# Kernel optimization log

Measured on AMD Instinct MI355X. Metric: run time of the kernel, lower is better.

The kernel has to match this reference:

```python
import jax, jax.numpy as jnp
import numpy as np
import math

NUM_SECTORS = 8
HIDDEN = 128
FEAT = 64
MAX_DIST = 10.0


def gru_last(x, Wih, Whh, bih, bhh):
    # PyTorch GRU (gate order r,z,n); x: (B,T,D) -> last hidden (B,H)
    B = x.shape[0]
    H = Whh.shape[1]
    xp = jnp.einsum('btd,gd->btg', x, Wih) + bih  # (B,T,3H)

    def step(h, xpt):
        hp = h @ Whh.T + bhh
        xr, xz, xn = jnp.split(xpt, 3, -1)
        hr, hz, hn = jnp.split(hp, 3, -1)
        r = jax.nn.sigmoid(xr + hr)
        z = jax.nn.sigmoid(xz + hz)
        n = jnp.tanh(xn + r * hn)
        h_new = (1.0 - z) * n + z * h
        return h_new, None

    h0 = jnp.zeros((B, H), x.dtype)
    hT, _ = jax.lax.scan(step, h0, jnp.swapaxes(xp, 0, 1))
    return hT


def setup_inputs() -> dict:
    key = jax.random.key(0)
    ks = iter(jax.random.split(key, 32))
    B, N, T = 2048, 64, 8
    H, Hn = HIDDEN, HIDDEN // 2
    s = 0.05

    def p(shape):
        return jax.random.normal(next(ks), shape, jnp.float32) * s

    inp = {
        'target_trajectory': jax.random.normal(next(ks), (B, T, 2), jnp.float32),
        'neighbor_trajectories': jax.random.normal(next(ks), (B, N, T, 2), jnp.float32),
        'relative_angles': jax.random.uniform(next(ks), (B, N), jnp.float32) * (2.0 * math.pi),
        'neighbor_mask': (jax.random.uniform(next(ks), (B, N)) > 0.2).astype(jnp.float32),
        # target GRU (H=128)
        'Wih_t': p((3 * H, 2)), 'Whh_t': p((3 * H, H)), 'bih_t': p((3 * H,)), 'bhh_t': p((3 * H,)),
        # neighbor GRU (H=64)
        'Wih_n': p((3 * Hn, 2)), 'Whh_n': p((3 * Hn, Hn)), 'bih_n': p((3 * Hn,)), 'bhh_n': p((3 * Hn,)),
        # sector encoder: 68 -> 128 -> 128
        'W1': p((H, 4 + Hn)), 'b1': p((H,)), 'W2': p((H, H)), 'b2': p((H,)),
        # fusion: 1152 -> 256 -> 128 -> 64
        'Wf1': p((2 * H, H + NUM_SECTORS * H)), 'bf1': p((2 * H,)),
        'Wf2': p((H, 2 * H)), 'bf2': p((H,)),
        'Wf3': p((FEAT, H)), 'bf3': p((FEAT,)),
        'ln_g': jnp.ones((FEAT,), jnp.float32), 'ln_b': jnp.zeros((FEAT,), jnp.float32),
    }
    return inp


def reference(target_trajectory, neighbor_trajectories, relative_angles, neighbor_mask,
              Wih_t, Whh_t, bih_t, bhh_t, Wih_n, Whh_n, bih_n, bhh_n,
              W1, b1, W2, b2, Wf1, bf1, Wf2, bf2, Wf3, bf3, ln_g, ln_b):
    B, N, T, D = neighbor_trajectories.shape
    S = NUM_SECTORS

    # trajectory encoders
    target_feature = gru_last(target_trajectory, Wih_t, Whh_t, bih_t, bhh_t)  # (B,128)
    nf = gru_last(neighbor_trajectories.reshape(B * N, T, D), Wih_n, Whh_n, bih_n, bhh_n)
    nf = nf.reshape(B, N, -1)  # (B,N,64)

    # geometry
    target_pos = target_trajectory[:, -1, :]                      # (B,2)
    npos = neighbor_trajectories[:, :, -1, :]                     # (B,N,2)
    dist = jnp.linalg.norm(npos - target_pos[:, None, :], axis=-1)  # (B,N)
    vel = neighbor_trajectories[:, :, -1, :] - neighbor_trajectories[:, :, -2, :]  # (B,N,2)

    # sector assignment (vectorized segment reduce over sectors)
    sector_size = 2.0 * math.pi / S
    sid = jnp.clip((relative_angles / sector_size).astype(jnp.int32), 0, S - 1)  # (B,N)
    valid = neighbor_mask > 0
    memb = ((sid[..., None] == jnp.arange(S)) & valid[..., None]).astype(dist.dtype)  # (B,N,S)

    count = memb.sum(1)                        # (B,S)
    nonempty = count > 0
    safe = jnp.maximum(count, 1.0)
    avg_d = jnp.where(nonempty, (dist[..., None] * memb).sum(1) / safe, 0.0)  # (B,S)
    avg_v = jnp.where(nonempty[..., None], jnp.einsum('bns,bnc->bsc', memb, vel) / safe[..., None], 0.0)

    w = jnp.exp(-dist / MAX_DIST)              # (B,N)
    wm = w[..., None] * memb                   # (B,N,S)
    wsum = wm.sum(1) + 1e-8                    # (B,S)
    wfeat = jnp.einsum('bns,bnh->bsh', wm, nf) / wsum[..., None]  # (B,S,64)

    sector_feats = jnp.concatenate([count[..., None], avg_d[..., None], avg_v, wfeat], axis=-1)  # (B,S,68)

    # sector encoder MLP (dropout off / eval)
    h = jax.nn.relu(sector_feats @ W1.T + b1)
    h = jax.nn.relu(h @ W2.T + b2)             # (B,S,128)
    enc = h.reshape(B, S * HIDDEN)

    combined = jnp.concatenate([target_feature, enc], axis=-1)  # (B,1152)
    f = jax.nn.relu(combined @ Wf1.T + bf1)
    f = jax.nn.relu(f @ Wf2.T + bf2)
    f = jax.nn.relu(f @ Wf3.T + bf3)           # (B,64)

    mu = f.mean(-1, keepdims=True)
    var = ((f - mu) ** 2).mean(-1, keepdims=True)
    return (f - mu) / jnp.sqrt(var + 1e-5) * ln_g + ln_b
```

## Files before the change

### kernel.cpp

```cpp
#include <hip/hip_runtime.h>

typedef __attribute__((ext_vector_type(8))) short short8;
typedef __attribute__((ext_vector_type(4))) float f32x4;

#define SGC (-1.44269504088896341f)
#define THC ( 2.88539008177792681f)

__device__ __forceinline__ unsigned short f2bf(float f){
  unsigned u = __float_as_uint(f);
  return (unsigned short)((u + 0x7fffu + ((u >> 16) & 1u)) >> 16);
}
__device__ __forceinline__ float bf2f(unsigned short b){
  return __uint_as_float(((unsigned)b) << 16);
}
__device__ __forceinline__ unsigned f2bf_cvt(float f){
  unsigned r;
  asm("v_cvt_pk_bf16_f32 %0, %1, %1" : "=v"(r) : "v"(f));
  return r;
}
__device__ __forceinline__ unsigned f2bf_pk(float lo, float hi){
  unsigned r;
  asm("v_cvt_pk_bf16_f32 %0, %1, %2" : "=v"(r) : "v"(lo), "v"(hi));
  return r;
}

__global__ __launch_bounds__(256) void k_prep(
    const float* __restrict__ Whh_t, const float* __restrict__ W1,
    const float* __restrict__ W2,    const float* __restrict__ Wf1,
    const float* __restrict__ Wf2,   const float* __restrict__ Wf3,
    const float* __restrict__ Whh_n,
    unsigned short* __restrict__ wgt)
{
  int i = blockIdx.x * 256 + threadIdx.x;
  if (i < 49152){
    int g = i >> 7;
    float s = (g < 256) ? SGC : THC;
    wgt[i] = f2bf(Whh_t[i] * s); return;
  }
  i -= 49152;
  if (i < 12288){ int r = i / 96, c = i % 96;
    wgt[49152 + i] = (c < 68) ? f2bf(W1[r*68 + c]) : (unsigned short)0; return; }
  i -= 12288;
  if (i < 16384){ wgt[61440 + i] = f2bf(W2[i]); return; }
  i -= 16384;
  if (i < 294912){ wgt[77824 + i] = f2bf(Wf1[i]); return; }
  i -= 294912;
  if (i < 32768){ wgt[372736 + i] = f2bf(Wf2[i]); return; }
  i -= 32768;
  if (i < 8192){ wgt[405504 + i] = f2bf(Wf3[i]); return; }
  i -= 8192;
  if (i < 12288){
    int g = i >> 6;
    float s = (g < 128) ? SGC : THC;
    wgt[413696 + i] = f2bf(Whh_n[i] * s); return;
  }
}

__global__ __launch_bounds__(256, 4) void k_gru_n(
    const float* __restrict__ ttraj, const float* __restrict__ ntraj,
    const float* __restrict__ rang,  const float* __restrict__ nmask,
    const float* __restrict__ Wih_n,
    const float* __restrict__ bih_n, const float* __restrict__ bhh_n,
    const unsigned short* __restrict__ wgt,
    unsigned short* __restrict__ sf)
{
  __shared__ char smem[38912];
  const int tid = threadIdx.x;
  const int w = tid >> 6, u = (tid >> 4) & 3, c = tid & 15;
  const int b = blockIdx.x;
  const unsigned short* whhN_b = wgt + 413696;

  unsigned short* whh2 = (unsigned short*)smem;
  unsigned short* wx   = whh2 + 12288;
  unsigned short* hall = (unsigned short*)(smem + 27648);
  unsigned short* hb   = hall + w * 1152;
  unsigned* xpk = (unsigned*)(smem + 36864);
  float* pool   = (float*)(smem + 36864);

  for (int i = tid; i < 1536; i += 256){
    int nt = i >> 7, rem = i & 127;
    int hf = rem >> 6, uu = (rem >> 4) & 3, cc = rem & 15;
    *(short8*)&whh2[nt*1024 + hf*512 + (uu*16+cc)*8] =
        *(const short8*)&whhN_b[(nt*16+cc)*64 + hf*32 + uu*8];
  }
  if (tid < 192){
    int t = tid >> 4, cc = tid & 15;
    float s = (t < 8) ? SGC : THC;
    int g = (t < 4) ? (t*16 + cc) : (t < 8) ? (64 + (t-4)*16 + cc) : (128 + (t-8)*16 + cc);
    float bsum = (t < 8) ? (bih_n[g] + bhh_n[g]) : bih_n[g];
    unsigned short* p = &wx[t*128 + cc*8];
    *(short8*)p = (short8){0,0,0,0,0,0,0,0};
    p[0] = f2bf(Wih_n[g*2]   * s);
    p[1] = f2bf(Wih_n[g*2+1] * s);
    p[2] = f2bf(bsum * s);
  }
  {
    float4 v = ((const float4*)(ntraj + (size_t)b * 1024))[tid];
    int n = tid >> 2, p = (tid & 3) * 2;
    xpk[p*64 + n]       = f2bf_pk(v.x, v.y);
    xpk[(p+1)*64 + n]   = f2bf_pk(v.z, v.w);
  }
  __syncthreads();

  short8 BX[12];
#pragma unroll
  for (int t = 0; t < 12; ++t) BX[t] = *(const short8*)&wx[t*128 + c*8];

  float bh_[4];
#pragma unroll
  for (int gt = 0; gt < 4; ++gt) bh_[gt] = bhh_n[128 + gt*16 + c] * THC;

  float hcur[4][4];
#pragma unroll
  for (int gt=0; gt<4; ++gt)
#pragma unroll
    for (int q=0; q<4; ++q) hcur[gt][q] = 0.0f;

  auto gates = [&](int gt, const f32x4& aR, const f32x4& aZ, const f32x4& aN, const f32x4& aX){
#pragma unroll
    for (int q = 0; q < 4; ++q){
      float r = __builtin_amdgcn_rcpf(1.0f + __builtin_amdgcn_exp2f(aR[q]));
      float z = __builtin_amdgcn_rcpf(1.0f + __builtin_amdgcn_exp2f(aZ[q]));
      float hn = aN[q] + bh_[gt];
      float pn = __builtin_fmaf(r, hn, aX[q]);
      float E = __builtin_amdgcn_exp2f(pn);
      float n = __builtin_fmaf(-2.0f, __builtin_amdgcn_rcpf(E + 1.0f), 1.0f);
      float hnew = __builtin_fmaf(z, hcur[gt][q] - n, n);
      hcur[gt][q] = hnew;
      hb[(u*4+q)*72 + gt*16 + c] = (unsigned short)f2bf_cvt(hnew);
    }
  };

  const int lane8 = (u*16 + c) * 8;
  const f32x4 zz = {0.f,0.f,0.f,0.f};

  for (int st = 0; st < 8; ++st){
    unsigned p01 = xpk[st*64 + w*16 + c];
    bool u0 = (u == 0);
    union { unsigned ui[4]; short8 s8; } a2u;
    a2u.ui[0] = u0 ? p01 : 0u;
    a2u.ui[1] = u0 ? 0x3F80u : 0u;
    a2u.ui[2] = 0u; a2u.ui[3] = 0u;
    short8 a2 = a2u.s8;

    if (st > 0){
      short8 a0 = *(short8*)&hb[c*72 + u*8];
      short8 a1 = *(short8*)&hb[c*72 + 32 + u*8];
#pragma unroll
      for (int gt = 0; gt < 4; ++gt){
        const unsigned short* pr = whh2 + gt*1024 + lane8;
        const unsigned short* pz = whh2 + (4+gt)*1024 + lane8;
        const unsigned short* pq = whh2 + (8+gt)*1024 + lane8;
        f32x4 aR = __builtin_amdgcn_mfma_f32_16x16x32_bf16(a0, *(const short8*)pr, zz, 0,0,0);
        aR = __builtin_amdgcn_mfma_f32_16x16x32_bf16(a1, *(const short8*)(pr+512), aR, 0,0,0);
        aR = __builtin_amdgcn_mfma_f32_16x16x32_bf16(a2, BX[gt], aR, 0,0,0);
        f32x4 aZ = __builtin_amdgcn_mfma_f32_16x16x32_bf16(a0, *(const short8*)pz, zz, 0,0,0);
        aZ = __builtin_amdgcn_mfma_f32_16x16x32_bf16(a1, *(const short8*)(pz+512), aZ, 0,0,0);
        aZ = __builtin_amdgcn_mfma_f32_16x16x32_bf16(a2, BX[4+gt], aZ, 0,0,0);
        f32x4 aN = __builtin_amdgcn_mfma_f32_16x16x32_bf16(a0, *(const short8*)pq, zz, 0,0,0);
        aN = __builtin_amdgcn_mfma_f32_16x16x32_bf16(a1, *(const short8*)(pq+512), aN, 0,0,0);
        f32x4 aX = __builtin_amdgcn_mfma_f32_16x16x32_bf16(a2, BX[8+gt], zz, 0,0,0);
        gates(gt, aR, aZ, aN, aX);
      }
    } else {
#pragma unroll
      for (int gt = 0; gt < 4; ++gt){
        f32x4 aR = __builtin_amdgcn_mfma_f32_16x16x32_bf16(a2, BX[gt], zz, 0,0,0);
        f32x4 aZ = __builtin_amdgcn_mfma_f32_16x16x32_bf16(a2, BX[4+gt], zz, 0,0,0);
        f32x4 aX = __builtin_amdgcn_mfma_f32_16x16x32_bf16(a2, BX[8+gt], zz, 0,0,0);
        gates(gt, aR, aZ, zz, aX);
      }
    }
  }
  __syncthreads();

  if (tid < 64){
    int n = tid;
    const float* nb = ntraj + (size_t)b*1024 + n*16;
    float px = nb[14], py = nb[15];
    float vx = px - nb[12], vy = py - nb[13];
    float m   = nmask[(size_t)b*64 + n];
    float ang = rang[(size_t)b*64 + n];
    float tx = ttraj[(size_t)b*16 + 14], ty = ttraj[(size_t)b*16 + 15];
    float dx = px - tx, dy = py - ty;
    float dist = __builtin_amdgcn_sqrtf(dx*dx + dy*dy);
    int sid = (int)(ang / 0.78539816339744830962f);
    sid = sid < 0 ? 0 : (sid > 7 ? 7 : sid);
    bool valid = m > 0.0f;
    float wv = valid ? __builtin_amdgcn_exp2f(dist * -0.14426950408889634f) : 0.0f;
    pool[n]       = valid ? dist : 0.0f;
    pool[64 + n]  = valid ? vx   : 0.0f;
    pool[128 + n] = valid ? vy   : 0.0f;
    pool[192 + n] = wv;
    pool[256 + n] = valid ? (float)sid : -1.0f;
  }
  __syncthreads();
  if (tid < 8){
    int s = tid;
    float cnt=0.f, sd=0.f, sx=0.f, sy=0.f, sw=0.f;
    for (int n=0; n<64; ++n){
      if (pool[256+n] == (float)s){
        cnt += 1.f; sd += pool[n]; sx += pool[64+n]; sy += pool[128+n]; sw += pool[192+n];
      }
    }
    float inv = (cnt > 0.f) ? __builtin_amdgcn_rcpf(cnt) : 0.f;
    pool[320 + s] = cnt;
    pool[328 + s] = sd * inv;
    pool[336 + s] = sx * inv;
    pool[344 + s] = sy * inv;
    pool[352 + s] = __builtin_amdgcn_rcpf(sw + 1e-8f);
  }
  __syncthreads();
#pragma unroll
  for (int rep = 0; rep < 2; ++rep){
    int p = tid + rep*256;
    int s = p >> 6, h = p & 63;
    float fs = (float)s;
    float a = 0.f;
    for (int n = 0; n < 64; ++n){
      float wmv = (pool[256+n] == fs) ? pool[192+n] : 0.f;
      float nf  = bf2f(hall[(n>>4)*1152 + (n&15)*72 + h]);
      a += wmv * nf;
    }
    sf[((size_t)b*8 + s)*96 + 4 + h] = (unsigned short)f2bf_cvt(a * pool[352+s]);
  }
  if (tid < 32){
    int s = tid >> 2, cc = tid & 3;
    sf[((size_t)b*8 + s)*96 + cc] = (unsigned short)f2bf_cvt(pool[320 + cc*8 + s]);
  }
  if (tid < 224){
    int s = tid / 28, cc = 68 + tid % 28;
    sf[((size_t)b*8 + s)*96 + cc] = 0;
  }
}

__global__ __launch_bounds__(256) void k_gru_t(
    const float* __restrict__ ttraj,
    const float* __restrict__ Wih_t, const float* __restrict__ bih_t, const float* __restrict__ bhh_t,
    const unsigned short* __restrict__ wgt,
    unsigned short* __restrict__ combined)
{
  __shared__ char smem[9728];
  const int tid = threadIdx.x, w = tid >> 6, u = (tid >> 4) & 3, c = tid & 15;
  unsigned short* hb0 = (unsigned short*)smem;
  unsigned short* hb1 = (unsigned short*)(smem + 4352);
  float* xs = (float*)(smem + 8704);

  xs[tid] = ttraj[(size_t)blockIdx.x*256 + tid];

  int ntg[6];
  ntg[0] = 2*w; ntg[1] = 2*w+1;
  ntg[2] = 8+2*w; ntg[3] = 9+2*w;
  ntg[4] = 16+2*w; ntg[5] = 17+2*w;

  short8 Bf[6][4];
#pragma unroll
  for (int lt2 = 0; lt2 < 6; ++lt2){
    const unsigned short* wp = wgt + (ntg[lt2]*16 + c)*128 + u*8;
#pragma unroll
    for (int kk = 0; kk < 4; ++kk)
      Bf[lt2][kk] = *(const short8*)(wp + kk*32);
  }

  float Wr0[2],Wr1[2],BR[2],Wz0[2],Wz1[2],BZ[2],Wn0[2],Wn1[2],BI[2],BH[2];
#pragma unroll
  for (int gt = 0; gt < 2; ++gt){
    int g = w*32 + gt*16 + c;
    Wr0[gt]=Wih_t[g*2]*SGC;        Wr1[gt]=Wih_t[g*2+1]*SGC;        BR[gt]=(bih_t[g]+bhh_t[g])*SGC;
    Wz0[gt]=Wih_t[(128+g)*2]*SGC;  Wz1[gt]=Wih_t[(128+g)*2+1]*SGC;  BZ[gt]=(bih_t[128+g]+bhh_t[128+g])*SGC;
    Wn0[gt]=Wih_t[(256+g)*2]*THC;  Wn1[gt]=Wih_t[(256+g)*2+1]*THC;  BI[gt]=bih_t[256+g]*THC; BH[gt]=bhh_t[256+g]*THC;
  }
  float hcur[2][4];
#pragma unroll
  for (int gt=0; gt<2; ++gt)
#pragma unroll
    for (int q=0; q<4; ++q) hcur[gt][q] = 0.0f;
  __syncthreads();

  for (int st = 0; st < 8; ++st){
    unsigned short* rbuf = (st & 1) ? hb0 : hb1;
    unsigned short* wbuf = (st & 1) ? hb1 : hb0;
    f32x4 acc[6];
    if (st > 0){
      short8 a0 = *(short8*)&rbuf[c*136 + u*8];
      short8 a1 = *(short8*)&rbuf[c*136 + 32 + u*8];
      short8 a2 = *(short8*)&rbuf[c*136 + 64 + u*8];
      short8 a3 = *(short8*)&rbuf[c*136 + 96 + u*8];
#pragma unroll
      for (int lt2 = 0; lt2 < 6; ++lt2){
        f32x4 t = {0.f,0.f,0.f,0.f};
        t = __builtin_amdgcn_mfma_f32_16x16x32_bf16(a0, Bf[lt2][0], t, 0,0,0);
        t = __builtin_amdgcn_mfma_f32_16x16x32_bf16(a1, Bf[lt2][1], t, 0,0,0);
        t = __builtin_amdgcn_mfma_f32_16x16x32_bf16(a2, Bf[lt2][2], t, 0,0,0);
        acc[lt2] = __builtin_amdgcn_mfma_f32_16x16x32_bf16(a3, Bf[lt2][3], t, 0,0,0);
      }
    } else {
#pragma unroll
      for (int lt2 = 0; lt2 < 6; ++lt2) acc[lt2] = (f32x4){0.f,0.f,0.f,0.f};
    }
#pragma unroll
    for (int gt = 0; gt < 2; ++gt){
#pragma unroll
      for (int q = 0; q < 4; ++q){
        int sq = u*4 + q;
        float x0 = xs[sq*16 + st*2], x1 = xs[sq*16 + st*2 + 1];
        float rp = __builtin_fmaf(Wr0[gt], x0, __builtin_fmaf(Wr1[gt], x1, acc[gt][q] + BR[gt]));
        float zp = __builtin_fmaf(Wz0[gt], x0, __builtin_fmaf(Wz1[gt], x1, acc[2+gt][q] + BZ[gt]));
        float r = __builtin_amdgcn_rcpf(1.0f + __builtin_amdgcn_exp2f(rp));
        float z = __builtin_amdgcn_rcpf(1.0f + __builtin_amdgcn_exp2f(zp));
        float hnv = acc[4+gt][q] + BH[gt];
        float pn = __builtin_fmaf(Wn0[gt], x0, __builtin_fmaf(Wn1[gt], x1, __builtin_fmaf(r, hnv, BI[gt])));
        float E = __builtin_amdgcn_exp2f(pn);
        float n = __builtin_fmaf(-2.0f, __builtin_amdgcn_rcpf(E + 1.0f), 1.0f);
        float hnew = __builtin_fmaf(z, hcur[gt][q] - n, n);
        hcur[gt][q] = hnew;
        if (st < 7){
          wbuf[sq*136 + w*32 + gt*16 + c] = (unsigned short)f2bf_cvt(hnew);
        } else {
          int row = blockIdx.x*16 + sq;
          combined[(size_t)row*1152 + w*32 + gt*16 + c] = (unsigned short)f2bf_cvt(hnew);
        }
      }
    }
    if (st < 7) __syncthreads();
  }
}

__global__ __launch_bounds__(256) void k_mlp12(
    const unsigned short* __restrict__ sf,
    const unsigned short* __restrict__ wgt,
    const float* __restrict__ b1, const float* __restrict__ b2,
    unsigned short* __restrict__ combined)
{
  __shared__ char smem[18432];
  unsigned short* hb = (unsigned short*)smem + (threadIdx.x >> 6) * 2176;
  float* b1s = (float*)(smem + 17408);
  float* b2s = b1s + 128;
  const unsigned short* w1b = wgt + 49152;
  const unsigned short* w2b = wgt + 61440;
  const int tid = threadIdx.x, w = tid >> 6, u = (tid >> 4) & 3, c = tid & 15;
  if (tid < 128){ b1s[tid] = b1[tid]; b2s[tid] = b2[tid]; }
  __syncthreads();
  const int rowb = blockIdx.x * 64 + w * 16;

  f32x4 acc[8];
#pragma unroll
  for (int nt=0; nt<8; ++nt) acc[nt] = (f32x4){0.f,0.f,0.f,0.f};
#pragma unroll
  for (int kc=0; kc<3; ++kc){
    short8 a = *(const short8*)&sf[(size_t)(rowb + c)*96 + kc*32 + u*8];
#pragma unroll
    for (int nt=0; nt<8; ++nt){
      short8 bb = *(const short8*)&w1b[(nt*16+c)*96 + kc*32 + u*8];
      acc[nt] = __builtin_amdgcn_mfma_f32_16x16x32_bf16(a, bb, acc[nt], 0,0,0);
    }
  }
#pragma unroll
  for (int nt=0; nt<8; ++nt){
    float bias = b1s[nt*16+c];
#pragma unroll
    for (int q=0; q<4; ++q){
      float v = acc[nt][q] + bias; v = v > 0.f ? v : 0.f;
      hb[(u*4+q)*136 + nt*16 + c] = (unsigned short)f2bf_cvt(v);
    }
  }
  f32x4 acc2[8];
#pragma unroll
  for (int nt=0; nt<8; ++nt) acc2[nt] = (f32x4){0.f,0.f,0.f,0.f};
#pragma unroll
  for (int kc=0; kc<4; ++kc){
    short8 a = *(short8*)&hb[c*136 + kc*32 + u*8];
#pragma unroll
    for (int nt=0; nt<8; ++nt){
      short8 bb = *(const short8*)&w2b[(nt*16+c)*128 + kc*32 + u*8];
      acc2[nt] = __builtin_amdgcn_mfma_f32_16x16x32_bf16(a, bb, acc2[nt], 0,0,0);
    }
  }
#pragma unroll
  for (int nt=0; nt<8; ++nt){
    float bias = b2s[nt*16+c];
#pragma unroll
    for (int q=0; q<4; ++q){
      float v = acc2[nt][q] + bias; v = v > 0.f ? v : 0.f;
      int r = rowb + u*4 + q;
      combined[(size_t)(r >> 3)*1152 + 128 + (r & 7)*128 + nt*16 + c] = (unsigned short)f2bf_cvt(v);
    }
  }
}

__global__ __launch_bounds__(256) void k_head(
    const unsigned short* __restrict__ combined,
    const unsigned short* __restrict__ wgt,
    const float* __restrict__ bf1, const float* __restrict__ bf2, const float* __restrict__ bf3,
    const float* __restrict__ lng, const float* __restrict__ lnb,
    float* __restrict__ out)
{
  __shared__ char smem[15104];
  const int tid = threadIdx.x, w = tid >> 6, u = (tid >> 4) & 3, c = tid & 15;
  unsigned short* f1b = (unsigned short*)smem;
  unsigned short* f2b = (unsigned short*)(smem + 8448);
  float* bf1s = (float*)(smem + 12800); float* bf2s = (float*)(smem + 13824);
  float* bf3s = (float*)(smem + 14336);
  float* lngs = (float*)(smem + 14592); float* lnbs = (float*)(smem + 14848);
  const unsigned short* wf1b = wgt + 77824;
  const unsigned short* wf2b = wgt + 372736;
  const unsigned short* wf3b = wgt + 405504;
  bf1s[tid] = bf1[tid];
  if (tid < 128) bf2s[tid] = bf2[tid];
  if (tid < 64){ bf3s[tid] = bf3[tid]; lngs[tid] = lng[tid]; lnbs[tid] = lnb[tid]; }
  __syncthreads();
  const int rowb = blockIdx.x * 16;

  f32x4 acc[4];
#pragma unroll
  for (int i=0; i<4; ++i) acc[i] = (f32x4){0.f,0.f,0.f,0.f};
#pragma unroll 4
  for (int kc=0; kc<36; ++kc){
    short8 a = *(const short8*)&combined[(size_t)(rowb + c)*1152 + kc*32 + u*8];
#pragma unroll
    for (int i=0; i<4; ++i){
      int nt = w*4 + i;
      short8 bb = *(const short8*)&wf1b[(size_t)(nt*16+c)*1152 + kc*32 + u*8];
      acc[i] = __builtin_amdgcn_mfma_f32_16x16x32_bf16(a, bb, acc[i], 0,0,0);
    }
  }
#pragma unroll
  for (int i=0; i<4; ++i){
    int nt = w*4 + i;
    float bias = bf1s[nt*16+c];
#pragma unroll
    for (int q=0; q<4; ++q){
      float v = acc[i][q] + bias; v = v > 0.f ? v : 0.f;
      f1b[(u*4+q)*264 + nt*16 + c] = (unsigned short)f2bf_cvt(v);
    }
  }
  __syncthreads();

  f32x4 acc2[2];
#pragma unroll
  for (int i=0; i<2; ++i) acc2[i] = (f32x4){0.f,0.f,0.f,0.f};
#pragma unroll
  for (int kc=0; kc<8; ++kc){
    short8 a = *(short8*)&f1b[c*264 + kc*32 + u*8];
#pragma unroll
    for (int i=0; i<2; ++i){
      int nt = w*2 + i;
      short8 bb = *(const short8*)&wf2b[(nt*16+c)*256 + kc*32 + u*8];
      acc2[i] = __builtin_amdgcn_mfma_f32_16x16x32_bf16(a, bb, acc2[i], 0,0,0);
    }
  }
#pragma unroll
  for (int i=0; i<2; ++i){
    int nt = w*2 + i;
    float bias = bf2s[nt*16+c];
#pragma unroll
    for (int q=0; q<4; ++q){
      float v = acc2[i][q] + bias; v = v > 0.f ? v : 0.f;
      f2b[(u*4+q)*136 + nt*16 + c] = (unsigned short)f2bf_cvt(v);
    }
  }
  __syncthreads();

  f32x4 acc3[4];
#pragma unroll
  for (int nt=0; nt<4; ++nt) acc3[nt] = (f32x4){0.f,0.f,0.f,0.f};
#pragma unroll
  for (int kc=0; kc<4; ++kc){
    short8 a = *(short8*)&f2b[c*136 + kc*32 + u*8];
#pragma unroll
    for (int nt=0; nt<4; ++nt){
      short8 bb = *(const short8*)&wf3b[(nt*16+c)*128 + kc*32 + u*8];
      acc3[nt] = __builtin_amdgcn_mfma_f32_16x16x32_bf16(a, bb, acc3[nt], 0,0,0);
    }
  }
  if (w == 0){
    float v[4][4];
#pragma unroll
    for (int nt=0; nt<4; ++nt){
      float bias = bf3s[nt*16+c];
#pragma unroll
      for (int q=0; q<4; ++q){
        float t = acc3[nt][q] + bias; v[nt][q] = t > 0.f ? t : 0.f;
      }
    }
#pragma unroll
    for (int q=0; q<4; ++q){
      float p = v[0][q] + v[1][q] + v[2][q] + v[3][q];
      p += __shfl_xor(p, 1); p += __shfl_xor(p, 2); p += __shfl_xor(p, 4); p += __shfl_xor(p, 8);
      float mu = p * 0.015625f;
      float d0 = v[0][q]-mu, d1 = v[1][q]-mu, d2 = v[2][q]-mu, d3 = v[3][q]-mu;
      float p2 = d0*d0 + d1*d1 + d2*d2 + d3*d3;
      p2 += __shfl_xor(p2, 1); p2 += __shfl_xor(p2, 2); p2 += __shfl_xor(p2, 4); p2 += __shfl_xor(p2, 8);
      float rstd = __builtin_amdgcn_rsqf(p2 * 0.015625f + 1e-5f);
      int row = rowb + u*4 + q;
#pragma unroll
      for (int nt=0; nt<4; ++nt){
        int col = nt*16 + c;
        out[(size_t)row*64 + col] = (v[nt][q] - mu) * rstd * lngs[col] + lnbs[col];
      }
    }
  }
}

extern "C" void kernel_launch(void* const* d_in, const int* in_sizes, int n_in,
                              void* d_out, int out_size, void* d_ws, size_t ws_size,
                              hipStream_t stream)
{
  const float* ttraj = (const float*)d_in[0];
  const float* ntraj = (const float*)d_in[1];
  const float* rang  = (const float*)d_in[2];
  const float* nmask = (const float*)d_in[3];
  const float* Wih_t = (const float*)d_in[4];
  const float* Whh_t = (const float*)d_in[5];
  const float* bih_t = (const float*)d_in[6];
  const float* bhh_t = (const float*)d_in[7];
  const float* Wih_n = (const float*)d_in[8];
  const float* Whh_n = (const float*)d_in[9];
  const float* bih_n = (const float*)d_in[10];
  const float* bhh_n = (const float*)d_in[11];
  const float* W1  = (const float*)d_in[12];
  const float* b1  = (const float*)d_in[13];
  const float* W2  = (const float*)d_in[14];
  const float* b2  = (const float*)d_in[15];
  const float* Wf1 = (const float*)d_in[16];
  const float* bf1 = (const float*)d_in[17];
  const float* Wf2 = (const float*)d_in[18];
  const float* bf2 = (const float*)d_in[19];
  const float* Wf3 = (const float*)d_in[20];
  const float* bf3 = (const float*)d_in[21];
  const float* lng = (const float*)d_in[22];
  const float* lnb = (const float*)d_in[23];

  char* ws = (char*)d_ws;
  unsigned short* combined = (unsigned short*)ws;
  unsigned short* sf       = (unsigned short*)(ws + 5242880);
  unsigned short* wgt      = (unsigned short*)(ws + 8388608);

  hipLaunchKernelGGL(k_prep, dim3(1664), dim3(256), 0, stream,
                     Whh_t, W1, W2, Wf1, Wf2, Wf3, Whh_n, wgt);
  hipLaunchKernelGGL(k_gru_n, dim3(2048), dim3(256), 0, stream,
                     ttraj, ntraj, rang, nmask, Wih_n, bih_n, bhh_n, wgt, sf);
  hipLaunchKernelGGL(k_gru_t, dim3(128), dim3(256), 0, stream,
                     ttraj, Wih_t, bih_t, bhh_t, wgt, combined);
  hipLaunchKernelGGL(k_mlp12, dim3(256), dim3(256), 0, stream, sf, wgt, b1, b2, combined);
  hipLaunchKernelGGL(k_head, dim3(128), dim3(256), 0, stream,
                     combined, wgt, bf1, bf2, bf3, lng, lnb, (float*)d_out);
}
```

Baseline: 135.1 us.

## Fuse sector-encoder MLP into neighbor GRU kernel and drop k_mlp12

Moves the sector encoder (68->128->128 MLP) into the per-batch neighbor GRU kernel, keeping sector features and the first hidden layer in shared memory (aliasing the no-longer-needed Whh buffer) instead of round-tripping through global memory and launching a separate kernel. Each block now runs a tiny 8-row MFMA (half the 16-row tile wasted) with weights read from global per block. It also replaces the register-cached input-projection weights (BX) with per-step LDS reads and disables unrolling of the timestep loops to reduce register pressure. The fused kernel does extra work per block and adds two barriers.

Measured after the change: 139.8 us. 1.04x slower.

```diff
diff --git a/kernel.cpp b/kernel.cpp
--- a/kernel.cpp
+++ b/kernel.cpp
@@ -62,7 +62,8 @@
     const float* __restrict__ Wih_n,
     const float* __restrict__ bih_n, const float* __restrict__ bhh_n,
     const unsigned short* __restrict__ wgt,
-    unsigned short* __restrict__ sf)
+    const float* __restrict__ b1, const float* __restrict__ b2,
+    unsigned short* __restrict__ combined)
 {
   __shared__ char smem[38912];
   const int tid = threadIdx.x;
@@ -76,6 +77,8 @@
   unsigned short* hb   = hall + w * 1152;
   unsigned* xpk = (unsigned*)(smem + 36864);
   float* pool   = (float*)(smem + 36864);
+  unsigned short* sfl = whh2;
+  unsigned short* h1l = whh2 + 1536;
 
   for (int i = tid; i < 1536; i += 256){
     int nt = i >> 7, rem = i & 127;
@@ -102,10 +105,6 @@
   }
   __syncthreads();
 
-  short8 BX[12];
-#pragma unroll
-  for (int t = 0; t < 12; ++t) BX[t] = *(const short8*)&wx[t*128 + c*8];
-
   float bh_[4];
 #pragma unroll
   for (int gt = 0; gt < 4; ++gt) bh_[gt] = bhh_n[128 + gt*16 + c] * THC;
@@ -134,6 +133,7 @@
   const int lane8 = (u*16 + c) * 8;
   const f32x4 zz = {0.f,0.f,0.f,0.f};
 
+#pragma unroll 1
   for (int st = 0; st < 8; ++st){
     unsigned p01 = xpk[st*64 + w*16 + c];
     bool u0 = (u == 0);
@@ -151,29 +151,36 @@
         const unsigned short* pr = whh2 + gt*1024 + lane8;
         const unsigned short* pz = whh2 + (4+gt)*1024 + lane8;
         const unsigned short* pq = whh2 + (8+gt)*1024 + lane8;
+        short8 bxr = *(const short8*)&wx[gt*128 + c*8];
+        short8 bxz = *(const short8*)&wx[(4+gt)*128 + c*8];
+        short8 bxn = *(const short8*)&wx[(8+gt)*128 + c*8];
         f32x4 aR = __builtin_amdgcn_mfma_f32_16x16x32_bf16(a0, *(const short8*)pr, zz, 0,0,0);
         aR = __builtin_amdgcn_mfma_f32_16x16x32_bf16(a1, *(const short8*)(pr+512), aR, 0,0,0);
-        aR = __builtin_amdgcn_mfma_f32_16x16x32_bf16(a2, BX[gt], aR, 0,0,0);
+        aR = __builtin_amdgcn_mfma_f32_16x16x32_bf16(a2, bxr, aR, 0,0,0);
         f32x4 aZ = __builtin_amdgcn_mfma_f32_16x16x32_bf16(a0, *(const short8*)pz, zz, 0,0,0);
         aZ = __builtin_amdgcn_mfma_f32_16x16x32_bf16(a1, *(const short8*)(pz+512), aZ, 0,0,0);
-        aZ = __builtin_amdgcn_mfma_f32_16x16x32_bf16(a2, BX[4+gt], aZ, 0,0,0);
+        aZ = __builtin_amdgcn_mfma_f32_16x16x32_bf16(a2, bxz, aZ, 0,0,0);
         f32x4 aN = __builtin_amdgcn_mfma_f32_16x16x32_bf16(a0, *(const short8*)pq, zz, 0,0,0);
         aN = __builtin_amdgcn_mfma_f32_16x16x32_bf16(a1, *(const short8*)(pq+512), aN, 0,0,0);
-        f32x4 aX = __builtin_amdgcn_mfma_f32_16x16x32_bf16(a2, BX[8+gt], zz, 0,0,0);
+        f32x4 aX = __builtin_amdgcn_mfma_f32_16x16x32_bf16(a2, bxn, zz, 0,0,0);
         gates(gt, aR, aZ, aN, aX);
       }
     } else {
 #pragma unroll
       for (int gt = 0; gt < 4; ++gt){
-        f32x4 aR = __builtin_amdgcn_mfma_f32_16x16x32_bf16(a2, BX[gt], zz, 0,0,0);
-        f32x4 aZ = __builtin_amdgcn_mfma_f32_16x16x32_bf16(a2, BX[4+gt], zz, 0,0,0);
-        f32x4 aX = __builtin_amdgcn_mfma_f32_16x16x32_bf16(a2, BX[8+gt], zz, 0,0,0);
+        short8 bxr = *(const short8*)&wx[gt*128 + c*8];
+        short8 bxz = *(const short8*)&wx[(4+gt)*128 + c*8];
+        short8 bxn = *(const short8*)&wx[(8+gt)*128 + c*8];
+        f32x4 aR = __builtin_amdgcn_mfma_f32_16x16x32_bf16(a2, bxr, zz, 0,0,0);
+        f32x4 aZ = __builtin_amdgcn_mfma_f32_16x16x32_bf16(a2, bxz, zz, 0,0,0);
+        f32x4 aX = __builtin_amdgcn_mfma_f32_16x16x32_bf16(a2, bxn, zz, 0,0,0);
         gates(gt, aR, aZ, zz, aX);
       }
     }
   }
   __syncthreads();
 
+  for (int i = tid; i < 1536; i += 256) sfl[i] = 0;
   if (tid < 64){
     int n = tid;
     const float* nb = ntraj + (size_t)b*1024 + n*16;
@@ -198,6 +205,7 @@
   if (tid < 8){
     int s = tid;
     float cnt=0.f, sd=0.f, sx=0.f, sy=0.f, sw=0.f;
+#pragma unroll 4
     for (int n=0; n<64; ++n){
       if (pool[256+n] == (float)s){
         cnt += 1.f; sd += pool[n]; sx += pool[64+n]; sy += pool[128+n]; sw += pool[192+n];
@@ -217,20 +225,73 @@
     int s = p >> 6, h = p & 63;
     float fs = (float)s;
     float a = 0.f;
+#pragma unroll 4
     for (int n = 0; n < 64; ++n){
       float wmv = (pool[256+n] == fs) ? pool[192+n] : 0.f;
       float nf  = bf2f(hall[(n>>4)*1152 + (n&15)*72 + h]);
       a += wmv * nf;
     }
-    sf[((size_t)b*8 + s)*96 + 4 + h] = (unsigned short)f2bf_cvt(a * pool[352+s]);
+    sfl[s*96 + 4 + h] = (unsigned short)f2bf_cvt(a * pool[352+s]);
   }
   if (tid < 32){
     int s = tid >> 2, cc = tid & 3;
-    sf[((size_t)b*8 + s)*96 + cc] = (unsigned short)f2bf_cvt(pool[320 + cc*8 + s]);
-  }
-  if (tid < 224){
-    int s = tid / 28, cc = 68 + tid % 28;
-    sf[((size_t)b*8 + s)*96 + cc] = 0;
+    sfl[s*96 + cc] = (unsigned short)f2bf_cvt(pool[320 + cc*8 + s]);
+  }
+  __syncthreads();
+
+  const unsigned short* w1b = wgt + 49152;
+  const unsigned short* w2b = wgt + 61440;
+  f32x4 accA[2];
+#pragma unroll
+  for (int i=0;i<2;++i) accA[i] = zz;
+#pragma unroll
+  for (int kc=0; kc<3; ++kc){
+    short8 a = (short8){0,0,0,0,0,0,0,0};
+    if (c < 8) a = *(const short8*)&sfl[c*96 + kc*32 + u*8];
+#pragma unroll
+    for (int i=0;i<2;++i){
+      int nt = w*2 + i;
+      short8 bb = *(const short8*)&w1b[(nt*16+c)*96 + kc*32 + u*8];
+      accA[i] = __builtin_amdgcn_mfma_f32_16x16x32_bf16(a, bb, accA[i], 0,0,0);
+    }
+  }
+#pragma unroll
+  for (int i=0;i<2;++i){
+    int nt = w*2 + i;
+    float bias = b1[nt*16 + c];
+#pragma unroll
+    for (int q=0;q<4;++q){
+      float v = accA[i][q] + bias; v = v > 0.f ? v : 0.f;
+      h1l[(u*4+q)*136 + nt*16 + c] = (unsigned short)f2bf_cvt(v);
+    }
+  }
+  __syncthreads();
+
+  f32x4 accB[2];
+#pragma unroll
+  for (int i=0;i<2;++i) accB[i] = zz;
+#pragma unroll
+  for (int kc=0; kc<4; ++kc){
+    short8 a = *(short8*)&h1l[c*136 + kc*32 + u*8];
+#pragma unroll
+    for (int i=0;i<2;++i){
+      int nt = w*2 + i;
+      short8 bb = *(const short8*)&w2b[(nt*16+c)*128 + kc*32 + u*8];
+      accB[i] = __builtin_amdgcn_mfma_f32_16x16x32_bf16(a, bb, accB[i], 0,0,0);
+    }
+  }
+#pragma unroll
+  for (int i=0;i<2;++i){
+    int nt = w*2 + i;
+    float bias = b2[nt*16 + c];
+#pragma unroll
+    for (int q=0;q<4;++q){
+      int row = u*4 + q;
+      if (row < 8){
+        float v = accB[i][q] + bias; v = v > 0.f ? v : 0.f;
+        combined[(size_t)b*1152 + 128 + row*128 + nt*16 + c] = (unsigned short)f2bf_cvt(v);
+      }
+    }
   }
 }
 
@@ -277,6 +338,7 @@
     for (int q=0; q<4; ++q) hcur[gt][q] = 0.0f;
   __syncthreads();
 
+#pragma unroll 1
   for (int st = 0; st < 8; ++st){
     unsigned short* rbuf = (st & 1) ? hb0 : hb1;
     unsigned short* wbuf = (st & 1) ? hb1 : hb0;
@@ -323,68 +385,6 @@
       }
     }
     if (st < 7) __syncthreads();
-  }
-}
-
-__global__ __launch_bounds__(256) void k_mlp12(
-    const unsigned short* __restrict__ sf,
-    const unsigned short* __restrict__ wgt,
-    const float* __restrict__ b1, const float* __restrict__ b2,
-    unsigned short* __restrict__ combined)
-{
-  __shared__ char smem[18432];
-  unsigned short* hb = (unsigned short*)smem + (threadIdx.x >> 6) * 2176;
-  float* b1s = (float*)(smem + 17408);
-  float* b2s = b1s + 128;
-  const unsigned short* w1b = wgt + 49152;
-  const unsigned short* w2b = wgt + 61440;
-  const int tid = threadIdx.x, w = tid >> 6, u = (tid >> 4) & 3, c = tid & 15;
-  if (tid < 128){ b1s[tid] = b1[tid]; b2s[tid] = b2[tid]; }
-  __syncthreads();
-  const int rowb = blockIdx.x * 64 + w * 16;
-
-  f32x4 acc[8];
-#pragma unroll
-  for (int nt=0; nt<8; ++nt) acc[nt] = (f32x4){0.f,0.f,0.f,0.f};
-#pragma unroll
-  for (int kc=0; kc<3; ++kc){
-    short8 a = *(const short8*)&sf[(size_t)(rowb + c)*96 + kc*32 + u*8];
-#pragma unroll
-    for (int nt=0; nt<8; ++nt){
-      short8 bb = *(const short8*)&w1b[(nt*16+c)*96 + kc*32 + u*8];
-      acc[nt] = __builtin_amdgcn_mfma_f32_16x16x32_bf16(a, bb, acc[nt], 0,0,0);
-    }
-  }
-#pragma unroll
-  for (int nt=0; nt<8; ++nt){
-    float bias = b1s[nt*16+c];
-#pragma unroll
-    for (int q=0; q<4; ++q){
-      float v = acc[nt][q] + bias; v = v > 0.f ? v : 0.f;
-      hb[(u*4+q)*136 + nt*16 + c] = (unsigned short)f2bf_cvt(v);
-    }
-  }
-  f32x4 acc2[8];
-#pragma unroll
-  for (int nt=0; nt<8; ++nt) acc2[nt] = (f32x4){0.f,0.f,0.f,0.f};
-#pragma unroll
-  for (int kc=0; kc<4; ++kc){
-    short8 a = *(short8*)&hb[c*136 + kc*32 + u*8];
-#pragma unroll
-    for (int nt=0; nt<8; ++nt){
-      short8 bb = *(const short8*)&w2b[(nt*16+c)*128 + kc*32 + u*8];
-      acc2[nt] = __builtin_amdgcn_mfma_f32_16x16x32_bf16(a, bb, acc2[nt], 0,0,0);
-    }
-  }
-#pragma unroll
-  for (int nt=0; nt<8; ++nt){
-    float bias = b2s[nt*16+c];
-#pragma unroll
-    for (int q=0; q<4; ++q){
-      float v = acc2[nt][q] + bias; v = v > 0.f ? v : 0.f;
-      int r = rowb + u*4 + q;
-      combined[(size_t)(r >> 3)*1152 + 128 + (r & 7)*128 + nt*16 + c] = (unsigned short)f2bf_cvt(v);
-    }
   }
 }
 
@@ -533,16 +533,14 @@
 
   char* ws = (char*)d_ws;
   unsigned short* combined = (unsigned short*)ws;
-  unsigned short* sf       = (unsigned short*)(ws + 5242880);
   unsigned short* wgt      = (unsigned short*)(ws + 8388608);
 
   hipLaunchKernelGGL(k_prep, dim3(1664), dim3(256), 0, stream,
                      Whh_t, W1, W2, Wf1, Wf2, Wf3, Whh_n, wgt);
   hipLaunchKernelGGL(k_gru_n, dim3(2048), dim3(256), 0, stream,
-                     ttraj, ntraj, rang, nmask, Wih_n, bih_n, bhh_n, wgt, sf);
+                     ttraj, ntraj, rang, nmask, Wih_n, bih_n, bhh_n, wgt, b1, b2, combined);
   hipLaunchKernelGGL(k_gru_t, dim3(128), dim3(256), 0, stream,
                      ttraj, Wih_t, bih_t, bhh_t, wgt, combined);
-  hipLaunchKernelGGL(k_mlp12, dim3(256), dim3(256), 0, stream, sf, wgt, b1, b2, combined);
   hipLaunchKernelGGL(k_head, dim3(128), dim3(256), 0, stream,
                      combined, wgt, bf1, bf2, bf3, lng, lnb, (float*)d_out);
 }
```

## Keep neighbor GRU weights in registers and split hidden units across waves

Applied to the files above, without the earlier changes.

The neighbor GRU kernel now assigns each wave a 16-column slice of hidden units across all 64 neighbors. Each wave keeps its slice of recurrent and input weights in registers loaded once from global memory, so the per-block copy of the weights into shared memory goes away. The input-projection weights and biases are prebuilt in the prep kernel. Shared memory drops from about 38 KB to 11 KB, which should allow more resident blocks, at the cost of two block-wide barriers per timestep for the shared hidden state.

Measured after the change: 138.2 us. +2.4%, slower.

```diff
diff --git a/kernel.cpp b/kernel.cpp
--- a/kernel.cpp
+++ b/kernel.cpp
@@ -28,7 +28,8 @@
     const float* __restrict__ Whh_t, const float* __restrict__ W1,
     const float* __restrict__ W2,    const float* __restrict__ Wf1,
     const float* __restrict__ Wf2,   const float* __restrict__ Wf3,
-    const float* __restrict__ Whh_n,
+    const float* __restrict__ Whh_n, const float* __restrict__ Wih_n,
+    const float* __restrict__ bih_n, const float* __restrict__ bhh_n,
     unsigned short* __restrict__ wgt)
 {
   int i = blockIdx.x * 256 + threadIdx.x;
@@ -54,125 +55,112 @@
     float s = (g < 128) ? SGC : THC;
     wgt[413696 + i] = f2bf(Whh_n[i] * s); return;
   }
+  i -= 12288;
+  if (i < 1536){
+    int t = i >> 7, rem = i & 127, cc = rem >> 3, j = rem & 7;
+    float s = (t < 8) ? SGC : THC;
+    int g = (t < 4) ? (t*16 + cc) : (t < 8) ? (64 + (t-4)*16 + cc) : (128 + (t-8)*16 + cc);
+    float v = 0.f;
+    if (j == 0) v = Wih_n[g*2]   * s;
+    if (j == 1) v = Wih_n[g*2+1] * s;
+    if (j == 2) v = ((t < 8) ? (bih_n[g] + bhh_n[g]) : bih_n[g]) * s;
+    wgt[425984 + i] = f2bf(v); return;
+  }
 }
 
 __global__ __launch_bounds__(256, 4) void k_gru_n(
     const float* __restrict__ ttraj, const float* __restrict__ ntraj,
     const float* __restrict__ rang,  const float* __restrict__ nmask,
-    const float* __restrict__ Wih_n,
-    const float* __restrict__ bih_n, const float* __restrict__ bhh_n,
+    const float* __restrict__ bhh_n,
     const unsigned short* __restrict__ wgt,
     unsigned short* __restrict__ sf)
 {
-  __shared__ char smem[38912];
+  __shared__ char smem[11264];
   const int tid = threadIdx.x;
   const int w = tid >> 6, u = (tid >> 4) & 3, c = tid & 15;
   const int b = blockIdx.x;
   const unsigned short* whhN_b = wgt + 413696;
-
-  unsigned short* whh2 = (unsigned short*)smem;
-  unsigned short* wx   = whh2 + 12288;
-  unsigned short* hall = (unsigned short*)(smem + 27648);
-  unsigned short* hb   = hall + w * 1152;
-  unsigned* xpk = (unsigned*)(smem + 36864);
-  float* pool   = (float*)(smem + 36864);
-
-  for (int i = tid; i < 1536; i += 256){
-    int nt = i >> 7, rem = i & 127;
-    int hf = rem >> 6, uu = (rem >> 4) & 3, cc = rem & 15;
-    *(short8*)&whh2[nt*1024 + hf*512 + (uu*16+cc)*8] =
-        *(const short8*)&whhN_b[(nt*16+cc)*64 + hf*32 + uu*8];
-  }
-  if (tid < 192){
-    int t = tid >> 4, cc = tid & 15;
-    float s = (t < 8) ? SGC : THC;
-    int g = (t < 4) ? (t*16 + cc) : (t < 8) ? (64 + (t-4)*16 + cc) : (128 + (t-8)*16 + cc);
-    float bsum = (t < 8) ? (bih_n[g] + bhh_n[g]) : bih_n[g];
-    unsigned short* p = &wx[t*128 + cc*8];
-    *(short8*)p = (short8){0,0,0,0,0,0,0,0};
-    p[0] = f2bf(Wih_n[g*2]   * s);
-    p[1] = f2bf(Wih_n[g*2+1] * s);
-    p[2] = f2bf(bsum * s);
-  }
+  const unsigned short* wxg    = wgt + 425984;
+
+  unsigned short* hbuf = (unsigned short*)smem;
+  unsigned* xpk = (unsigned*)(smem + 9216);
+  float* pool   = (float*)(smem + 9216);
+
+  short8 Bh[6], Bx[3];
+#pragma unroll
+  for (int k = 0; k < 3; ++k){
+    int nt = k*4 + w;
+    Bh[k*2+0] = *(const short8*)&whhN_b[(nt*16 + c)*64 + u*8];
+    Bh[k*2+1] = *(const short8*)&whhN_b[(nt*16 + c)*64 + 32 + u*8];
+    Bx[k]     = *(const short8*)&wxg[nt*128 + c*8];
+  }
+  const float bh_ = bhh_n[128 + w*16 + c] * THC;
+
   {
     float4 v = ((const float4*)(ntraj + (size_t)b * 1024))[tid];
     int n = tid >> 2, p = (tid & 3) * 2;
-    xpk[p*64 + n]       = f2bf_pk(v.x, v.y);
-    xpk[(p+1)*64 + n]   = f2bf_pk(v.z, v.w);
-  }
-  __syncthreads();
-
-  short8 BX[12];
-#pragma unroll
-  for (int t = 0; t < 12; ++t) BX[t] = *(const short8*)&wx[t*128 + c*8];
-
-  float bh_[4];
-#pragma unroll
-  for (int gt = 0; gt < 4; ++gt) bh_[gt] = bhh_n[128 + gt*16 + c] * THC;
+    xpk[p*64 + n]     = f2bf_pk(v.x, v.y);
+    xpk[(p+1)*64 + n] = f2bf_pk(v.z, v.w);
+  }
+  __syncthreads();
 
   float hcur[4][4];
 #pragma unroll
-  for (int gt=0; gt<4; ++gt)
-#pragma unroll
-    for (int q=0; q<4; ++q) hcur[gt][q] = 0.0f;
-
-  auto gates = [&](int gt, const f32x4& aR, const f32x4& aZ, const f32x4& aN, const f32x4& aX){
-#pragma unroll
-    for (int q = 0; q < 4; ++q){
-      float r = __builtin_amdgcn_rcpf(1.0f + __builtin_amdgcn_exp2f(aR[q]));
-      float z = __builtin_amdgcn_rcpf(1.0f + __builtin_amdgcn_exp2f(aZ[q]));
-      float hn = aN[q] + bh_[gt];
-      float pn = __builtin_fmaf(r, hn, aX[q]);
-      float E = __builtin_amdgcn_exp2f(pn);
-      float n = __builtin_fmaf(-2.0f, __builtin_amdgcn_rcpf(E + 1.0f), 1.0f);
-      float hnew = __builtin_fmaf(z, hcur[gt][q] - n, n);
-      hcur[gt][q] = hnew;
-      hb[(u*4+q)*72 + gt*16 + c] = (unsigned short)f2bf_cvt(hnew);
-    }
-  };
-
-  const int lane8 = (u*16 + c) * 8;
+  for (int sg=0; sg<4; ++sg)
+#pragma unroll
+    for (int q=0; q<4; ++q) hcur[sg][q] = 0.0f;
+
   const f32x4 zz = {0.f,0.f,0.f,0.f};
 
+#pragma unroll 1
   for (int st = 0; st < 8; ++st){
-    unsigned p01 = xpk[st*64 + w*16 + c];
-    bool u0 = (u == 0);
-    union { unsigned ui[4]; short8 s8; } a2u;
-    a2u.ui[0] = u0 ? p01 : 0u;
-    a2u.ui[1] = u0 ? 0x3F80u : 0u;
-    a2u.ui[2] = 0u; a2u.ui[3] = 0u;
-    short8 a2 = a2u.s8;
-
-    if (st > 0){
-      short8 a0 = *(short8*)&hb[c*72 + u*8];
-      short8 a1 = *(short8*)&hb[c*72 + 32 + u*8];
-#pragma unroll
-      for (int gt = 0; gt < 4; ++gt){
-        const unsigned short* pr = whh2 + gt*1024 + lane8;
-        const unsigned short* pz = whh2 + (4+gt)*1024 + lane8;
-        const unsigned short* pq = whh2 + (8+gt)*1024 + lane8;
-        f32x4 aR = __builtin_amdgcn_mfma_f32_16x16x32_bf16(a0, *(const short8*)pr, zz, 0,0,0);
-        aR = __builtin_amdgcn_mfma_f32_16x16x32_bf16(a1, *(const short8*)(pr+512), aR, 0,0,0);
-        aR = __builtin_amdgcn_mfma_f32_16x16x32_bf16(a2, BX[gt], aR, 0,0,0);
-        f32x4 aZ = __builtin_amdgcn_mfma_f32_16x16x32_bf16(a0, *(const short8*)pz, zz, 0,0,0);
-        aZ = __builtin_amdgcn_mfma_f32_16x16x32_bf16(a1, *(const short8*)(pz+512), aZ, 0,0,0);
-        aZ = __builtin_amdgcn_mfma_f32_16x16x32_bf16(a2, BX[4+gt], aZ, 0,0,0);
-        f32x4 aN = __builtin_amdgcn_mfma_f32_16x16x32_bf16(a0, *(const short8*)pq, zz, 0,0,0);
-        aN = __builtin_amdgcn_mfma_f32_16x16x32_bf16(a1, *(const short8*)(pq+512), aN, 0,0,0);
-        f32x4 aX = __builtin_amdgcn_mfma_f32_16x16x32_bf16(a2, BX[8+gt], zz, 0,0,0);
-        gates(gt, aR, aZ, aN, aX);
-      }
-    } else {
-#pragma unroll
-      for (int gt = 0; gt < 4; ++gt){
-        f32x4 aR = __builtin_amdgcn_mfma_f32_16x16x32_bf16(a2, BX[gt], zz, 0,0,0);
-        f32x4 aZ = __builtin_amdgcn_mfma_f32_16x16x32_bf16(a2, BX[4+gt], zz, 0,0,0);
-        f32x4 aX = __builtin_amdgcn_mfma_f32_16x16x32_bf16(a2, BX[8+gt], zz, 0,0,0);
-        gates(gt, aR, aZ, zz, aX);
-      }
-    }
-  }
-  __syncthreads();
+    short8 a0s[4], a1s[4];
+    unsigned xv[4];
+#pragma unroll
+    for (int sg = 0; sg < 4; ++sg){
+      xv[sg] = xpk[st*64 + sg*16 + c];
+      if (st > 0){
+        a0s[sg] = *(short8*)&hbuf[(sg*16 + c)*72 + u*8];
+        a1s[sg] = *(short8*)&hbuf[(sg*16 + c)*72 + 32 + u*8];
+      }
+    }
+    __syncthreads();
+
+#pragma unroll
+    for (int sg = 0; sg < 4; ++sg){
+      union { unsigned ui[4]; short8 s8; } a2u;
+      a2u.ui[0] = (u == 0) ? xv[sg] : 0u;
+      a2u.ui[1] = (u == 0) ? 0x3F80u : 0u;
+      a2u.ui[2] = 0u; a2u.ui[3] = 0u;
+      short8 a2 = a2u.s8;
+
+      f32x4 aR = __builtin_amdgcn_mfma_f32_16x16x32_bf16(a2, Bx[0], zz, 0,0,0);
+      f32x4 aZ = __builtin_amdgcn_mfma_f32_16x16x32_bf16(a2, Bx[1], zz, 0,0,0);
+      f32x4 aX = __builtin_amdgcn_mfma_f32_16x16x32_bf16(a2, Bx[2], zz, 0,0,0);
+      f32x4 aN = zz;
+      if (st > 0){
+        aR = __builtin_amdgcn_mfma_f32_16x16x32_bf16(a0s[sg], Bh[0], aR, 0,0,0);
+        aR = __builtin_amdgcn_mfma_f32_16x16x32_bf16(a1s[sg], Bh[1], aR, 0,0,0);
+        aZ = __builtin_amdgcn_mfma_f32_16x16x32_bf16(a0s[sg], Bh[2], aZ, 0,0,0);
+        aZ = __builtin_amdgcn_mfma_f32_16x16x32_bf16(a1s[sg], Bh[3], aZ, 0,0,0);
+        aN = __builtin_amdgcn_mfma_f32_16x16x32_bf16(a0s[sg], Bh[4], aN, 0,0,0);
+        aN = __builtin_amdgcn_mfma_f32_16x16x32_bf16(a1s[sg], Bh[5], aN, 0,0,0);
+      }
+#pragma unroll
+      for (int q = 0; q < 4; ++q){
+        float r = __builtin_amdgcn_rcpf(1.0f + __builtin_amdgcn_exp2f(aR[q]));
+        float z = __builtin_amdgcn_rcpf(1.0f + __builtin_amdgcn_exp2f(aZ[q]));
+        float hn = aN[q] + bh_;
+        float pn = __builtin_fmaf(r, hn, aX[q]);
+        float E = __builtin_amdgcn_exp2f(pn);
+        float n = __builtin_fmaf(-2.0f, __builtin_amdgcn_rcpf(E + 1.0f), 1.0f);
+        float hnew = __builtin_fmaf(z, hcur[sg][q] - n, n);
+        hcur[sg][q] = hnew;
+        hbuf[(sg*16 + u*4 + q)*72 + w*16 + c] = (unsigned short)f2bf_cvt(hnew);
+      }
+    }
+    __syncthreads();
+  }
 
   if (tid < 64){
     int n = tid;
@@ -198,6 +186,7 @@
   if (tid < 8){
     int s = tid;
     float cnt=0.f, sd=0.f, sx=0.f, sy=0.f, sw=0.f;
+#pragma unroll 4
     for (int n=0; n<64; ++n){
       if (pool[256+n] == (float)s){
         cnt += 1.f; sd += pool[n]; sx += pool[64+n]; sy += pool[128+n]; sw += pool[192+n];
@@ -217,9 +206,10 @@
     int s = p >> 6, h = p & 63;
     float fs = (float)s;
     float a = 0.f;
+#pragma unroll 4
     for (int n = 0; n < 64; ++n){
       float wmv = (pool[256+n] == fs) ? pool[192+n] : 0.f;
-      float nf  = bf2f(hall[(n>>4)*1152 + (n&15)*72 + h]);
+      float nf  = bf2f(hbuf[n*72 + h]);
       a += wmv * nf;
     }
     sf[((size_t)b*8 + s)*96 + 4 + h] = (unsigned short)f2bf_cvt(a * pool[352+s]);
@@ -277,6 +267,7 @@
     for (int q=0; q<4; ++q) hcur[gt][q] = 0.0f;
   __syncthreads();
 
+#pragma unroll 1
   for (int st = 0; st < 8; ++st){
     unsigned short* rbuf = (st & 1) ? hb0 : hb1;
     unsigned short* wbuf = (st & 1) ? hb1 : hb0;
@@ -536,10 +527,10 @@
   unsigned short* sf       = (unsigned short*)(ws + 5242880);
   unsigned short* wgt      = (unsigned short*)(ws + 8388608);
 
-  hipLaunchKernelGGL(k_prep, dim3(1664), dim3(256), 0, stream,
-                     Whh_t, W1, W2, Wf1, Wf2, Wf3, Whh_n, wgt);
+  hipLaunchKernelGGL(k_prep, dim3(1670), dim3(256), 0, stream,
+                     Whh_t, W1, W2, Wf1, Wf2, Wf3, Whh_n, Wih_n, bih_n, bhh_n, wgt);
   hipLaunchKernelGGL(k_gru_n, dim3(2048), dim3(256), 0, stream,
-                     ttraj, ntraj, rang, nmask, Wih_n, bih_n, bhh_n, wgt, sf);
+                     ttraj, ntraj, rang, nmask, bhh_n, wgt, sf);
   hipLaunchKernelGGL(k_gru_t, dim3(128), dim3(256), 0, stream,
                      ttraj, Wih_t, bih_t, bhh_t, wgt, combined);
   hipLaunchKernelGGL(k_mlp12, dim3(256), dim3(256), 0, stream, sf, wgt, b1, b2, combined);
```
